# Kernel tuning notes

Measured on AMD Instinct MI355X. Metric: run time of the kernel, lower is better.

The kernel has to match this reference:

```python
import jax, jax.numpy as jnp
import numpy as np

MASS = 0.5
G = 1.0  # constant offset -p[8]*g in the objective; does not affect argmin u*
NEWTON_ITERS = 30


def _lambertw(x):
    """Solve w*exp(w) = x for x >= 0 (principal branch) via Newton iterations."""
    w = jnp.log1p(x)  # good init on [0, inf)
    for _ in range(NEWTON_ITERS):
        ew = jnp.exp(w)
        w = w - (w * ew - x) / (ew * (w + 1.0))
    return w


def setup_inputs() -> dict:
    key = jax.random.key(0)
    kz, kt, k1, k2 = jax.random.split(key, 4)
    B, S, H = 500000, 12, 100
    return {
        "z": jax.random.normal(kz, (B, S), jnp.float32),
        "t": jax.random.uniform(kt, (B,), jnp.float32),
        "W1": jax.random.normal(k1, (S + 1, H), jnp.float32) * 0.1,
        "b1": jnp.zeros((H,), jnp.float32),
        "W2": jax.random.normal(k2, (H, S), jnp.float32) * 0.1,
        "b2": jnp.zeros((S,), jnp.float32),
    }


def reference(z, t, W1, b1, W2, b2):
    # p_net: MLP on concat([t, z])
    inp = jnp.concatenate([t[:, None], z], axis=1)          # [B, 13]
    h = jnp.tanh(inp @ W1 + b1)                              # [B, 100]
    p = h @ W2 + b2                                          # [B, 12]
    # Objective: c . u + exp(0.5*||u||^2) + const, with
    # c = [(p6+p7+p8)/m, p9, p10, p11]. Stationarity: c + u*exp(0.5||u||^2)=0
    # => u = -c*exp(-0.5*w), where w = ||u||^2 solves w*e^w = ||c||^2 (Lambert W).
    c = jnp.stack(
        [(p[:, 6] + p[:, 7] + p[:, 8]) / MASS, p[:, 9], p[:, 10], p[:, 11]],
        axis=1,
    )                                                        # [B, 4]
    x = jnp.sum(c * c, axis=1)                               # [B] = ||c||^2
    w = _lambertw(x)                                         # [B]
    ustar = -c * jnp.exp(-0.5 * w)[:, None]                  # [B, 4]
    return ustar
```

## Files before the change

### kernel.cpp

```cpp
#include <hip/hip_runtime.h>


constexpr int S = 12;
constexpr int H = 100;

__device__ __forceinline__ float fast_rcp(float x) {
    return __builtin_amdgcn_rcpf(x);
}

__device__ __forceinline__ float fast_tanh(float x) {
    float e = __expf(2.0f * x);
    return fmaf(-2.0f, fast_rcp(1.0f + e), 1.0f);
}

__global__ __launch_bounds__(256) void pack_weights(
    const float* __restrict__ W1, const float* __restrict__ b1,
    const float* __restrict__ W2, float* __restrict__ ws)
{
    int idx = blockIdx.x * 256 + threadIdx.x;
    if (idx < 1600) {
        int j = idx >> 4, k = idx & 15;
        float v = 0.0f;
        if (k < 13)       v = W1[k * H + j];
        else if (k == 13) v = b1[j];
        ws[idx] = v;
    } else if (idx < 2400) {
        int r = idx - 1600;
        int j = r >> 3, m = r & 7;
        ws[idx] = (m < 6) ? W2[j * S + 6 + m] : 0.0f;
    }
}

__global__ __launch_bounds__(256) void cvx_quad_kernel(
    const float* __restrict__ z, const float* __restrict__ t,
    const float* __restrict__ ws, const float* __restrict__ b2,
    float* __restrict__ out, int B)
{
    int i = blockIdx.x * 256 + threadIdx.x;
    if (i >= B) return;

    const float* W1T = ws;
    const float* W2P = ws + 1600;

    float inp[S + 1];
    inp[0] = t[i];
    const float4* zr = reinterpret_cast<const float4*>(z) + (size_t)i * 3;
    float4 a0 = zr[0], a1 = zr[1], a2 = zr[2];
    inp[1]  = a0.x; inp[2]  = a0.y; inp[3]  = a0.z; inp[4]  = a0.w;
    inp[5]  = a1.x; inp[6]  = a1.y; inp[7]  = a1.z; inp[8]  = a1.w;
    inp[9]  = a2.x; inp[10] = a2.y; inp[11] = a2.z; inp[12] = a2.w;

    float p0 = b2[6], p1 = b2[7], p2 = b2[8];
    float p3 = b2[9], p4 = b2[10], p5 = b2[11];

    #pragma unroll 2
    for (int j = 0; j < H; ++j) {
        const float4* wr = reinterpret_cast<const float4*>(W1T + j * 16);
        float4 wa = wr[0], wb = wr[1], wc = wr[2], wd = wr[3];
        float acc = wd.y;
        acc = fmaf(inp[0],  wa.x, acc);
        acc = fmaf(inp[1],  wa.y, acc);
        acc = fmaf(inp[2],  wa.z, acc);
        acc = fmaf(inp[3],  wa.w, acc);
        acc = fmaf(inp[4],  wb.x, acc);
        acc = fmaf(inp[5],  wb.y, acc);
        acc = fmaf(inp[6],  wb.z, acc);
        acc = fmaf(inp[7],  wb.w, acc);
        acc = fmaf(inp[8],  wc.x, acc);
        acc = fmaf(inp[9],  wc.y, acc);
        acc = fmaf(inp[10], wc.z, acc);
        acc = fmaf(inp[11], wc.w, acc);
        acc = fmaf(inp[12], wd.x, acc);

        float th = fast_tanh(acc);

        const float4* qr = reinterpret_cast<const float4*>(W2P + j * 8);
        float4 qa = qr[0], qb = qr[1];
        p0 = fmaf(th, qa.x, p0);
        p1 = fmaf(th, qa.y, p1);
        p2 = fmaf(th, qa.z, p2);
        p3 = fmaf(th, qa.w, p3);
        p4 = fmaf(th, qb.x, p4);
        p5 = fmaf(th, qb.y, p5);
    }

    float c0 = 2.0f * (p0 + p1 + p2);
    float c1 = p3, c2 = p4, c3 = p5;
    float x = fmaf(c0, c0, fmaf(c1, c1, fmaf(c2, c2, c3 * c3)));

    float w = __logf(1.0f + x);
    #pragma unroll
    for (int it = 0; it < 6; ++it) {
        float ew  = __expf(w);
        float num = fmaf(w, ew, -x);
        float den = fmaf(ew, w, ew);
        w = w - num * fast_rcp(den);
    }

    float sc = -__expf(-0.5f * w);
    float4 o;
    o.x = c0 * sc;
    o.y = c1 * sc;
    o.z = c2 * sc;
    o.w = c3 * sc;
    reinterpret_cast<float4*>(out)[i] = o;
}

extern "C" void kernel_launch(void* const* d_in, const int* in_sizes, int n_in,
                              void* d_out, int out_size, void* d_ws, size_t ws_size,
                              hipStream_t stream) {
    const float* z  = (const float*)d_in[0];
    const float* t  = (const float*)d_in[1];
    const float* W1 = (const float*)d_in[2];
    const float* b1 = (const float*)d_in[3];
    const float* W2 = (const float*)d_in[4];
    const float* b2 = (const float*)d_in[5];
    float* out = (float*)d_out;
    float* ws  = (float*)d_ws;

    pack_weights<<<dim3(10), dim3(256), 0, stream>>>(W1, b1, W2, ws);

    int B = in_sizes[1];
    int grid = (B + 255) / 256;
    cvx_quad_kernel<<<dim3(grid), dim3(256), 0, stream>>>(z, t, ws, b2, out, B);
}
```

Baseline: 118.7 us.

## Interleave hidden-unit pairs for packed float2 FMAs and prescale weights for exp2

Repacks W1, b1 and W2 so that each pair of hidden units sits interleaved, and rewrites the MLP loop to run on float2 values so the compiler can emit packed FP32 FMAs (v_pk_fma_f32) on CDNA. W1 and b1 are also prescaled by 2*log2(e), so tanh can use a raw exp2 with no multiply. The aim is to roughly halve the VALU instruction count of the dominant matmul. The cost is extra accumulator registers and a final horizontal add per output.

```diff
diff --git a/kernel.cpp b/kernel.cpp
--- a/kernel.cpp
+++ b/kernel.cpp
@@ -3,14 +3,14 @@
 
 constexpr int S = 12;
 constexpr int H = 100;
+#define TWO_LOG2E 2.8853900817779268f
 
 __device__ __forceinline__ float fast_rcp(float x) {
     return __builtin_amdgcn_rcpf(x);
 }
 
-__device__ __forceinline__ float fast_tanh(float x) {
-    float e = __expf(2.0f * x);
-    return fmaf(-2.0f, fast_rcp(1.0f + e), 1.0f);
+__device__ __forceinline__ float2 fma2(float2 a, float2 b, float2 c) {
+    return make_float2(fmaf(a.x, b.x, c.x), fmaf(a.y, b.y, c.y));
 }
 
 __global__ __launch_bounds__(256) void pack_weights(
@@ -19,15 +19,25 @@
 {
     int idx = blockIdx.x * 256 + threadIdx.x;
     if (idx < 1600) {
-        int j = idx >> 4, k = idx & 15;
+        int jp = idx >> 5, s = idx & 31;
         float v = 0.0f;
-        if (k < 13)       v = W1[k * H + j];
-        else if (k == 13) v = b1[j];
+        if (s < 26) {
+            int k = s >> 1, half = s & 1;
+            v = W1[k * H + 2 * jp + half] * TWO_LOG2E;
+        } else if (s < 28) {
+            int half = s & 1;
+            v = b1[2 * jp + half] * TWO_LOG2E;
+        }
         ws[idx] = v;
     } else if (idx < 2400) {
         int r = idx - 1600;
-        int j = r >> 3, m = r & 7;
-        ws[idx] = (m < 6) ? W2[j * S + 6 + m] : 0.0f;
+        int jp = r >> 4, s = r & 15;
+        float v = 0.0f;
+        if (s < 12) {
+            int m = s >> 1, half = s & 1;
+            v = W2[(2 * jp + half) * S + 6 + m];
+        }
+        ws[idx] = v;
     }
 }
 
@@ -39,9 +49,6 @@
     int i = blockIdx.x * 256 + threadIdx.x;
     if (i >= B) return;
 
-    const float* W1T = ws;
-    const float* W2P = ws + 1600;
-
     float inp[S + 1];
     inp[0] = t[i];
     const float4* zr = reinterpret_cast<const float4*>(z) + (size_t)i * 3;
@@ -50,39 +57,34 @@
     inp[5]  = a1.x; inp[6]  = a1.y; inp[7]  = a1.z; inp[8]  = a1.w;
     inp[9]  = a2.x; inp[10] = a2.y; inp[11] = a2.z; inp[12] = a2.w;
 
-    float p0 = b2[6], p1 = b2[7], p2 = b2[8];
-    float p3 = b2[9], p4 = b2[10], p5 = b2[11];
+    float2 p[6];
+    #pragma unroll
+    for (int m = 0; m < 6; ++m) p[m] = make_float2(b2[6 + m], 0.0f);
 
     #pragma unroll 2
-    for (int j = 0; j < H; ++j) {
-        const float4* wr = reinterpret_cast<const float4*>(W1T + j * 16);
-        float4 wa = wr[0], wb = wr[1], wc = wr[2], wd = wr[3];
-        float acc = wd.y;
-        acc = fmaf(inp[0],  wa.x, acc);
-        acc = fmaf(inp[1],  wa.y, acc);
-        acc = fmaf(inp[2],  wa.z, acc);
-        acc = fmaf(inp[3],  wa.w, acc);
-        acc = fmaf(inp[4],  wb.x, acc);
-        acc = fmaf(inp[5],  wb.y, acc);
-        acc = fmaf(inp[6],  wb.z, acc);
-        acc = fmaf(inp[7],  wb.w, acc);
-        acc = fmaf(inp[8],  wc.x, acc);
-        acc = fmaf(inp[9],  wc.y, acc);
-        acc = fmaf(inp[10], wc.z, acc);
-        acc = fmaf(inp[11], wc.w, acc);
-        acc = fmaf(inp[12], wd.x, acc);
+    for (int jp = 0; jp < H / 2; ++jp) {
+        const float2* wrow = reinterpret_cast<const float2*>(ws + jp * 32);
+        float2 acc = wrow[13];
+        #pragma unroll
+        for (int k = 0; k < S + 1; ++k) {
+            float2 ik = make_float2(inp[k], inp[k]);
+            acc = fma2(ik, wrow[k], acc);
+        }
+        float eA = __builtin_amdgcn_exp2f(acc.x);
+        float eB = __builtin_amdgcn_exp2f(acc.y);
+        float thA = fmaf(-2.0f, fast_rcp(1.0f + eA), 1.0f);
+        float thB = fmaf(-2.0f, fast_rcp(1.0f + eB), 1.0f);
+        float2 th = make_float2(thA, thB);
 
-        float th = fast_tanh(acc);
+        const float2* qrow = reinterpret_cast<const float2*>(ws + 1600 + jp * 16);
+        #pragma unroll
+        for (int m = 0; m < 6; ++m) {
+            p[m] = fma2(th, qrow[m], p[m]);
+        }
+    }
 
-        const float4* qr = reinterpret_cast<const float4*>(W2P + j * 8);
-        float4 qa = qr[0], qb = qr[1];
-        p0 = fmaf(th, qa.x, p0);
-        p1 = fmaf(th, qa.y, p1);
-        p2 = fmaf(th, qa.z, p2);
-        p3 = fmaf(th, qa.w, p3);
-        p4 = fmaf(th, qb.x, p4);
-        p5 = fmaf(th, qb.y, p5);
-    }
+    float p0 = p[0].x + p[0].y, p1 = p[1].x + p[1].y, p2 = p[2].x + p[2].y;
+    float p3 = p[3].x + p[3].y, p4 = p[4].x + p[4].y, p5 = p[5].x + p[5].y;
 
     float c0 = 2.0f * (p0 + p1 + p2);
     float c1 = p3, c2 = p4, c3 = p5;
```

Measured after the change: 113.0 us. 1.05x faster.
